# Performance work log

Hardware: AMD Instinct MI355X
Metric: run time of the kernel (lower is better)

Reference implementation:

```python
import jax, jax.numpy as jnp
import numpy as np

B, C, H = 32768, 1000, 128


def setup_inputs() -> dict:
    key = jax.random.key(0)
    ks = jax.random.split(key, 4)
    return {
        "logits": jax.random.normal(ks[0], (B, C), dtype=jnp.float32),
        "W1": jax.random.normal(ks[1], (C, H), dtype=jnp.float32) * 0.02,
        "b1": jnp.zeros((H,), dtype=jnp.float32),
        "W2": jax.random.normal(ks[2], (H, H), dtype=jnp.float32) * 0.02,
        "b2": jnp.zeros((H,), dtype=jnp.float32),
        "W3": jax.random.normal(ks[3], (H, C), dtype=jnp.float32) * 0.02,
        "b3": jnp.zeros((C,), dtype=jnp.float32),
    }


def reference(logits, W1, b1, W2, b2, W3, b3):
    prob = jax.nn.softmax(logits, axis=-1)                      # [B, C]
    # descending sort (torch.sort(descending=True))
    order = jnp.argsort(-prob, axis=-1)                          # [B, C] int
    sorted_prob = jnp.take_along_axis(prob, order, axis=-1)      # [B, C]
    # diffs between consecutive sorted probs, last slot = 1
    diffs = jnp.concatenate(
        [sorted_prob[:, :-1] - sorted_prob[:, 1:],
         jnp.ones((prob.shape[0], 1), dtype=prob.dtype)], axis=1)
    # adapter MLP on prob
    h = jax.nn.relu(prob @ W1 + b1)
    h = jax.nn.relu(h @ W2 + b2)
    cal = h @ W3 + b3                                            # [B, C]
    # sigmoid on all but the last column
    cal = jnp.concatenate([jax.nn.sigmoid(cal[:, :-1]), cal[:, -1:]], axis=1)
    v = diffs * cal                                              # [B, C]
    # S.T @ U @ v  ==  scatter(reverse-cumsum(v)) back to original order
    rev_cumsum = jnp.cumsum(v[:, ::-1], axis=1)[:, ::-1]         # suffix sum
    rows = jnp.arange(logits.shape[0])[:, None]
    fitted = jnp.zeros_like(logits).at[rows, order].set(rev_cumsum)
    return fitted + logits
```

## Files before the change

### kernel.cpp

```cpp
#include <hip/hip_runtime.h>
#include <hip/hip_bf16.h>

#define BROWS 32768
#define CDIM 1000
#define CPAD 1024
#define HDIM 128
#define REG 1056
#define WST  (2 * REG)
#define PHYS(i) ((i) + ((i) >> 5))

typedef __attribute__((ext_vector_type(8))) short short8;
typedef __attribute__((ext_vector_type(4))) float f32x4;

__device__ inline unsigned short f2bf(float x) {
    unsigned int b = __float_as_uint(x);
    unsigned int r = (b + 0x7FFFu + ((b >> 16) & 1u)) >> 16;
    return (unsigned short)r;
}
__device__ inline float bf2f(unsigned short u) {
    return __uint_as_float(((unsigned int)u) << 16);
}

__global__ __launch_bounds__(256) void k_prep(const float* __restrict__ W1,
                                              const float* __restrict__ W2,
                                              const float* __restrict__ W3,
                                              unsigned short* __restrict__ W1t,
                                              unsigned short* __restrict__ W2t,
                                              unsigned short* __restrict__ W3t) {
    const int idx = blockIdx.x * 256 + threadIdx.x;
    {
        const int n = idx >> 10, k = idx & 1023;
        W1t[idx] = (k < CDIM) ? f2bf(W1[(size_t)k * HDIM + n]) : (unsigned short)0;
    }
    {
        const int n = idx >> 7, k = idx & 127;
        W3t[idx] = (n < CDIM) ? f2bf(W3[(size_t)k * CDIM + n]) : (unsigned short)0;
    }
    if (idx < 16384) {
        const int n = idx >> 7, k = idx & 127;
        W2t[idx] = f2bf(W2[(size_t)k * HDIM + n]);
    }
}

__global__ __launch_bounds__(256) void k_softmax(const float* __restrict__ logits,
                                                 unsigned short* __restrict__ prob) {
    const int wv = threadIdx.x >> 6, lane = threadIdx.x & 63;
    const int row = (blockIdx.x << 2) + wv;
    const int base = lane << 4;
    const float* lrow = logits + (size_t)row * CDIM;
    float lg[16];
#pragma unroll
    for (int q = 0; q < 4; ++q) {
        const int c = base + (q << 2);
        if (c < CDIM) {
            const float4 v4 = *reinterpret_cast<const float4*>(lrow + c);
            lg[q * 4] = v4.x; lg[q * 4 + 1] = v4.y; lg[q * 4 + 2] = v4.z; lg[q * 4 + 3] = v4.w;
        } else {
            lg[q * 4] = lg[q * 4 + 1] = lg[q * 4 + 2] = lg[q * 4 + 3] = -INFINITY;
        }
    }
    float mx = lg[0];
#pragma unroll
    for (int e = 1; e < 16; ++e) mx = fmaxf(mx, lg[e]);
#pragma unroll
    for (int off = 32; off >= 1; off >>= 1) mx = fmaxf(mx, __shfl_xor(mx, off));
    float p[16], s = 0.f;
#pragma unroll
    for (int e = 0; e < 16; ++e) { p[e] = __expf(lg[e] - mx); s += p[e]; }
#pragma unroll
    for (int off = 32; off >= 1; off >>= 1) s += __shfl_xor(s, off);
    const float inv = 1.f / s;
    unsigned int w[8];
#pragma unroll
    for (int i = 0; i < 8; ++i) {
        const unsigned int lo = f2bf(p[2 * i] * inv);
        const unsigned int hi = f2bf(p[2 * i + 1] * inv);
        w[i] = lo | (hi << 16);
    }
    uint4 o0, o1;
    o0.x = w[0]; o0.y = w[1]; o0.z = w[2]; o0.w = w[3];
    o1.x = w[4]; o1.y = w[5]; o1.z = w[6]; o1.w = w[7];
    uint4* dst = reinterpret_cast<uint4*>(prob + (size_t)row * CPAD + base);
    dst[0] = o0; dst[1] = o1;
}

template <int EPI>
__global__ __launch_bounds__(512) void k_gemm(const unsigned short* __restrict__ A, int lda,
                                              const unsigned short* __restrict__ Bt, int ldb,
                                              const float* __restrict__ bias,
                                              unsigned short* __restrict__ outp, int ldo,
                                              int K, int nlimit) {
    __shared__ uint4 As[128 * 8];
    __shared__ uint4 Bs[128 * 8];
    const int tid = threadIdx.x;
    const int bm = blockIdx.x, bn = blockIdx.y;
    const int lane = tid & 63, w = tid >> 6;
    const int wm = (w >> 1) << 5;
    const int wn = (w & 1) << 6;
    const int l15 = lane & 15, l4 = lane >> 4;
    f32x4 acc[2][4] = {};

    for (int k0 = 0; k0 < K; k0 += 64) {
        __syncthreads();
#pragma unroll
        for (int i = 0; i < 2; ++i) {
            const int cid = tid + (i << 9);
            const int r = cid >> 3, c = cid & 7;
            As[(r << 3) + (c ^ (r & 7))] =
                *reinterpret_cast<const uint4*>(A + (size_t)(bm * 128 + r) * lda + k0 + (c << 3));
            Bs[(r << 3) + (c ^ (r & 7))] =
                *reinterpret_cast<const uint4*>(Bt + (size_t)(bn * 128 + r) * ldb + k0 + (c << 3));
        }
        __syncthreads();
#pragma unroll
        for (int kk = 0; kk < 2; ++kk) {
            short8 a[2], b[4];
#pragma unroll
            for (int mf = 0; mf < 2; ++mf) {
                const int r = wm + (mf << 4) + l15;
                a[mf] = *reinterpret_cast<const short8*>(&As[(r << 3) + (((kk << 2) + l4) ^ (r & 7))]);
            }
#pragma unroll
            for (int nf = 0; nf < 4; ++nf) {
                const int r = wn + (nf << 4) + l15;
                b[nf] = *reinterpret_cast<const short8*>(&Bs[(r << 3) + (((kk << 2) + l4) ^ (r & 7))]);
            }
#pragma unroll
            for (int mf = 0; mf < 2; ++mf)
#pragma unroll
                for (int nf = 0; nf < 4; ++nf)
                    acc[mf][nf] = __builtin_amdgcn_mfma_f32_16x16x32_bf16(a[mf], b[nf], acc[mf][nf], 0, 0, 0);
        }
    }
#pragma unroll
    for (int mf = 0; mf < 2; ++mf) {
#pragma unroll
        for (int nf = 0; nf < 4; ++nf) {
            const int n = (bn << 7) + wn + (nf << 4) + l15;
            float bv;
            if (EPI == 0) bv = bias[n];
            else bv = (n < nlimit) ? bias[n] : 0.f;
#pragma unroll
            for (int r = 0; r < 4; ++r) {
                const int m = (bm << 7) + wm + (mf << 4) + (l4 << 2) + r;
                float v = acc[mf][nf][r] + bv;
                if (EPI == 0) {
                    v = fmaxf(v, 0.f);
                } else {
                    if (n != nlimit - 1) v = 1.f / (1.f + __expf(-v));
                }
                outp[(size_t)m * ldo + n] = f2bf(v);
            }
        }
    }
}

__global__ __launch_bounds__(256) void k_sortfinish(const float* __restrict__ logits,
                                                    const unsigned short* __restrict__ cal,
                                                    float* __restrict__ out) {
    __shared__ unsigned int shm[4 * WST];
    const int wv = threadIdx.x >> 6, lane = threadIdx.x & 63;
    const int row = (blockIdx.x << 2) + wv;
    unsigned int* smA = &shm[wv * WST];
    unsigned int* smB = smA + REG;
    const int base = lane << 4;
    const int pb = base + (lane >> 1);

#pragma unroll
    for (int e = 0; e < 16; ++e) smA[pb + e] = 0u;

    const float* lrow = logits + (size_t)row * CDIM;
    float lg[16];
#pragma unroll
    for (int q = 0; q < 4; ++q) {
        const int c = base + (q << 2);
        if (c < CDIM) {
            const float4 v4 = *reinterpret_cast<const float4*>(lrow + c);
            lg[q * 4] = v4.x; lg[q * 4 + 1] = v4.y; lg[q * 4 + 2] = v4.z; lg[q * 4 + 3] = v4.w;
        } else {
            lg[q * 4] = lg[q * 4 + 1] = lg[q * 4 + 2] = lg[q * 4 + 3] = -INFINITY;
        }
    }
    const unsigned short* crow = cal + (size_t)row * CPAD + base;
    const uint4 c0v = *reinterpret_cast<const uint4*>(crow);
    const uint4 c1v = *reinterpret_cast<const uint4*>(crow + 8);

    float mx = lg[0];
#pragma unroll
    for (int e = 1; e < 16; ++e) mx = fmaxf(mx, lg[e]);
#pragma unroll
    for (int off = 32; off >= 1; off >>= 1) mx = fmaxf(mx, __shfl_xor(mx, off));
    float p[16], s = 0.f;
#pragma unroll
    for (int e = 0; e < 16; ++e) { p[e] = __expf(lg[e] - mx); s += p[e]; }
#pragma unroll
    for (int off = 32; off >= 1; off >>= 1) s += __shfl_xor(s, off);
    const float inv = 1.f / s;
#pragma unroll
    for (int e = 0; e < 16; ++e) p[e] *= inv;

    unsigned int key[16], offv[16];
#pragma unroll
    for (int e = 0; e < 16; ++e) {
        key[e] = __float_as_uint(p[e]) >> 20;
        offv[e] = (base + e < CDIM) ? atomicAdd(&smA[PHYS(key[e])], 1u) : 0u;
    }

    {
        unsigned int c16[16];
#pragma unroll
        for (int e = 0; e < 16; ++e) c16[e] = smA[pb + e];
        unsigned int lsum = 0;
#pragma unroll
        for (int e = 0; e < 16; ++e) lsum += c16[e];
        unsigned int suf = lsum;
#pragma unroll
        for (int off = 1; off < 64; off <<= 1) {
            const unsigned int u = __shfl_down(suf, off);
            if (lane + off < 64) suf += u;
        }
        unsigned int run = suf - lsum;
        unsigned int st[16];
#pragma unroll
        for (int e = 15; e >= 0; --e) { st[e] = run; run += c16[e]; }
#pragma unroll
        for (int e = 0; e < 16; ++e) smA[pb + e] = st[e];
    }

    int rk[16];
#pragma unroll
    for (int e = 0; e < 16; ++e)
        rk[e] = (base + e < CDIM) ? (int)(smA[PHYS(key[e])] + offv[e]) : 1023;

#pragma unroll
    for (int e = 0; e < 16; ++e)
        if (base + e < CDIM) smB[PHYS(rk[e])] = __float_as_uint(p[e]);

    float sp[16];
#pragma unroll
    for (int e = 0; e < 16; ++e) sp[e] = __uint_as_float(smB[pb + e]);
    const float spn_next = __shfl_down(sp[0], 1);
    const unsigned int cw[8] = {c0v.x, c0v.y, c0v.z, c0v.w, c1v.x, c1v.y, c1v.z, c1v.w};
    float v[16];
#pragma unroll
    for (int e = 0; e < 16; ++e) {
        const int r = base + e;
        const float cv = bf2f((unsigned short)((cw[e >> 1] >> ((e & 1) * 16)) & 0xFFFFu));
        const float spn = (e < 15) ? sp[e + 1] : spn_next;
        float val;
        if (r < CDIM - 1) val = (sp[e] - spn) * cv;
        else if (r == CDIM - 1) val = cv;
        else val = 0.f;
        v[e] = val;
    }
    float lsuf[16], run = 0.f;
#pragma unroll
    for (int e = 15; e >= 0; --e) { run += v[e]; lsuf[e] = run; }
    float pi = run;
#pragma unroll
    for (int off = 1; off < 64; off <<= 1) {
        const float u = __shfl_up(pi, off);
        if (lane >= off) pi += u;
    }
    const float tot = __shfl(pi, 63);
    const float after = tot - pi;

#pragma unroll
    for (int e = 0; e < 16; ++e) smA[pb + e] = __float_as_uint(lsuf[e] + after);
    float f[16];
#pragma unroll
    for (int e = 0; e < 16; ++e) f[e] = __uint_as_float(smA[PHYS(rk[e])]);
#pragma unroll
    for (int q = 0; q < 4; ++q) {
        const int c = base + (q << 2);
        if (c < CDIM) {
            float4 o;
            o.x = lg[q * 4] + f[q * 4];
            o.y = lg[q * 4 + 1] + f[q * 4 + 1];
            o.z = lg[q * 4 + 2] + f[q * 4 + 2];
            o.w = lg[q * 4 + 3] + f[q * 4 + 3];
            *reinterpret_cast<float4*>(out + (size_t)row * CDIM + c) = o;
        }
    }
}

extern "C" void kernel_launch(void* const* d_in, const int* in_sizes, int n_in,
                              void* d_out, int out_size, void* d_ws, size_t ws_size,
                              hipStream_t stream) {
    const float* logits = (const float*)d_in[0];
    const float* W1 = (const float*)d_in[1];
    const float* b1 = (const float*)d_in[2];
    const float* W2 = (const float*)d_in[3];
    const float* b2 = (const float*)d_in[4];
    const float* W3 = (const float*)d_in[5];
    const float* b3 = (const float*)d_in[6];
    float* out = (float*)d_out;

    char* ws = (char*)d_ws;
    unsigned short* prob = (unsigned short*)ws;
    unsigned short* h1   = (unsigned short*)(ws + 67108864);
    unsigned short* h2   = (unsigned short*)(ws + 75497472);
    unsigned short* W1t  = (unsigned short*)(ws + 83886080);
    unsigned short* W2t  = (unsigned short*)(ws + 84148224);
    unsigned short* W3t  = (unsigned short*)(ws + 84180992);
    unsigned short* cal  = prob;

    k_prep<<<512, 256, 0, stream>>>(W1, W2, W3, W1t, W2t, W3t);
    k_softmax<<<BROWS / 4, 256, 0, stream>>>(logits, prob);
    k_gemm<0><<<dim3(BROWS / 128, 1), 512, 0, stream>>>(prob, CPAD, W1t, CPAD, b1, h1, HDIM, CPAD, 0);
    k_gemm<0><<<dim3(BROWS / 128, 1), 512, 0, stream>>>(h1, HDIM, W2t, HDIM, b2, h2, HDIM, HDIM, 0);
    k_gemm<1><<<dim3(BROWS / 128, 8), 512, 0, stream>>>(h2, HDIM, W3t, HDIM, b3, cal, CPAD, HDIM, CDIM);
    k_sortfinish<<<BROWS / 4, 256, 0, stream>>>(logits, cal, out);
}
```

Measured before the change: 177.8 us.

## Fuse softmax into first GEMM A-load and compact calibration buffer

Replaces the softmax kernel that wrote a padded bf16 probability matrix with a row-statistics kernel that stores only the max and inverse sum per row. The first GEMM now reads fp32 logits directly and applies exp, normalize and bf16 conversion while staging A tiles into LDS. This removes the bf16 prob write and re-read at the cost of reading fp32 logits twice and doing more work in the GEMM load phase. The calibration buffer uses an unpadded CDIM stride, and the sort kernel reuses the stored row statistics and shares one LDS region between the histogram and the sorted probabilities, which halves its LDS use.

```diff
diff --git a/kernel.cpp b/kernel.cpp
--- a/kernel.cpp
+++ b/kernel.cpp
@@ -6,7 +6,6 @@
 #define CPAD 1024
 #define HDIM 128
 #define REG 1056
-#define WST  (2 * REG)
 #define PHYS(i) ((i) + ((i) >> 5))
 
 typedef __attribute__((ext_vector_type(8))) short short8;
@@ -42,8 +41,8 @@
     }
 }
 
-__global__ __launch_bounds__(256) void k_softmax(const float* __restrict__ logits,
-                                                 unsigned short* __restrict__ prob) {
+__global__ __launch_bounds__(256) void k_rowstat(const float* __restrict__ logits,
+                                                 float2* __restrict__ rstat) {
     const int wv = threadIdx.x >> 6, lane = threadIdx.x & 63;
     const int row = (blockIdx.x << 2) + wv;
     const int base = lane << 4;
@@ -64,24 +63,100 @@
     for (int e = 1; e < 16; ++e) mx = fmaxf(mx, lg[e]);
 #pragma unroll
     for (int off = 32; off >= 1; off >>= 1) mx = fmaxf(mx, __shfl_xor(mx, off));
-    float p[16], s = 0.f;
-#pragma unroll
-    for (int e = 0; e < 16; ++e) { p[e] = __expf(lg[e] - mx); s += p[e]; }
+    float s = 0.f;
+#pragma unroll
+    for (int e = 0; e < 16; ++e) s += __expf(lg[e] - mx);
 #pragma unroll
     for (int off = 32; off >= 1; off >>= 1) s += __shfl_xor(s, off);
-    const float inv = 1.f / s;
-    unsigned int w[8];
-#pragma unroll
-    for (int i = 0; i < 8; ++i) {
-        const unsigned int lo = f2bf(p[2 * i] * inv);
-        const unsigned int hi = f2bf(p[2 * i + 1] * inv);
-        w[i] = lo | (hi << 16);
-    }
-    uint4 o0, o1;
-    o0.x = w[0]; o0.y = w[1]; o0.z = w[2]; o0.w = w[3];
-    o1.x = w[4]; o1.y = w[5]; o1.z = w[6]; o1.w = w[7];
-    uint4* dst = reinterpret_cast<uint4*>(prob + (size_t)row * CPAD + base);
-    dst[0] = o0; dst[1] = o1;
+    if (lane == 0) rstat[row] = make_float2(mx, 1.f / s);
+}
+
+__global__ __launch_bounds__(512) void k_gemm1f(const float* __restrict__ logits,
+                                                const float2* __restrict__ rstat,
+                                                const unsigned short* __restrict__ W1t,
+                                                const float* __restrict__ b1,
+                                                unsigned short* __restrict__ h1) {
+    __shared__ uint4 As[128 * 8];
+    __shared__ uint4 Bs[128 * 8];
+    const int tid = threadIdx.x;
+    const int bm = blockIdx.x;
+    const int lane = tid & 63, w = tid >> 6;
+    const int wm = (w >> 1) << 5;
+    const int wn = (w & 1) << 6;
+    const int l15 = lane & 15, l4 = lane >> 4;
+    f32x4 acc[2][4] = {};
+
+    const int r = tid >> 2, q4 = tid & 3;
+    const float* lrowS = logits + (size_t)(bm * 128 + r) * CDIM;
+    const float2 st = rstat[bm * 128 + r];
+    const float mxv = st.x, invv = st.y;
+
+    for (int k0 = 0; k0 < CPAD; k0 += 64) {
+        __syncthreads();
+        {
+            unsigned int wd[8];
+#pragma unroll
+            for (int j = 0; j < 4; ++j) {
+                const int c = k0 + (q4 << 4) + (j << 2);
+                float p0 = 0.f, p1 = 0.f, p2 = 0.f, p3 = 0.f;
+                if (c < CDIM) {
+                    const float4 v4 = *reinterpret_cast<const float4*>(lrowS + c);
+                    p0 = __expf(v4.x - mxv) * invv;
+                    p1 = __expf(v4.y - mxv) * invv;
+                    p2 = __expf(v4.z - mxv) * invv;
+                    p3 = __expf(v4.w - mxv) * invv;
+                }
+                wd[2 * j]     = (unsigned int)f2bf(p0) | ((unsigned int)f2bf(p1) << 16);
+                wd[2 * j + 1] = (unsigned int)f2bf(p2) | ((unsigned int)f2bf(p3) << 16);
+            }
+            const int cc = q4 << 1;
+            uint4 u0, u1;
+            u0.x = wd[0]; u0.y = wd[1]; u0.z = wd[2]; u0.w = wd[3];
+            u1.x = wd[4]; u1.y = wd[5]; u1.z = wd[6]; u1.w = wd[7];
+            As[(r << 3) + (cc ^ (r & 7))] = u0;
+            As[(r << 3) + ((cc + 1) ^ (r & 7))] = u1;
+        }
+#pragma unroll
+        for (int i = 0; i < 2; ++i) {
+            const int cid = tid + (i << 9);
+            const int rb = cid >> 3, cb = cid & 7;
+            Bs[(rb << 3) + (cb ^ (rb & 7))] =
+                *reinterpret_cast<const uint4*>(W1t + (size_t)rb * CPAD + k0 + (cb << 3));
+        }
+        __syncthreads();
+#pragma unroll
+        for (int kk = 0; kk < 2; ++kk) {
+            short8 a[2], b[4];
+#pragma unroll
+            for (int mf = 0; mf < 2; ++mf) {
+                const int rr = wm + (mf << 4) + l15;
+                a[mf] = *reinterpret_cast<const short8*>(&As[(rr << 3) + (((kk << 2) + l4) ^ (rr & 7))]);
+            }
+#pragma unroll
+            for (int nf = 0; nf < 4; ++nf) {
+                const int rr = wn + (nf << 4) + l15;
+                b[nf] = *reinterpret_cast<const short8*>(&Bs[(rr << 3) + (((kk << 2) + l4) ^ (rr & 7))]);
+            }
+#pragma unroll
+            for (int mf = 0; mf < 2; ++mf)
+#pragma unroll
+                for (int nf = 0; nf < 4; ++nf)
+                    acc[mf][nf] = __builtin_amdgcn_mfma_f32_16x16x32_bf16(a[mf], b[nf], acc[mf][nf], 0, 0, 0);
+        }
+    }
+#pragma unroll
+    for (int mf = 0; mf < 2; ++mf) {
+#pragma unroll
+        for (int nf = 0; nf < 4; ++nf) {
+            const int n = wn + (nf << 4) + l15;
+            const float bv = b1[n];
+#pragma unroll
+            for (int rr = 0; rr < 4; ++rr) {
+                const int m = (bm << 7) + wm + (mf << 4) + (l4 << 2) + rr;
+                h1[(size_t)m * HDIM + n] = f2bf(fmaxf(acc[mf][nf][rr] + bv, 0.f));
+            }
+        }
+    }
 }
 
 template <int EPI>
@@ -137,9 +212,8 @@
 #pragma unroll
         for (int nf = 0; nf < 4; ++nf) {
             const int n = (bn << 7) + wn + (nf << 4) + l15;
-            float bv;
-            if (EPI == 0) bv = bias[n];
-            else bv = (n < nlimit) ? bias[n] : 0.f;
+            if (EPI == 1 && n >= nlimit) continue;
+            const float bv = bias[n];
 #pragma unroll
             for (int r = 0; r < 4; ++r) {
                 const int m = (bm << 7) + wm + (mf << 4) + (l4 << 2) + r;
@@ -156,13 +230,13 @@
 }
 
 __global__ __launch_bounds__(256) void k_sortfinish(const float* __restrict__ logits,
+                                                    const float2* __restrict__ rstat,
                                                     const unsigned short* __restrict__ cal,
                                                     float* __restrict__ out) {
-    __shared__ unsigned int shm[4 * WST];
+    __shared__ unsigned int shm[4 * REG];
     const int wv = threadIdx.x >> 6, lane = threadIdx.x & 63;
     const int row = (blockIdx.x << 2) + wv;
-    unsigned int* smA = &shm[wv * WST];
-    unsigned int* smB = smA + REG;
+    unsigned int* smA = &shm[wv * REG];
     const int base = lane << 4;
     const int pb = base + (lane >> 1);
 
@@ -181,23 +255,15 @@
             lg[q * 4] = lg[q * 4 + 1] = lg[q * 4 + 2] = lg[q * 4 + 3] = -INFINITY;
         }
     }
-    const unsigned short* crow = cal + (size_t)row * CPAD + base;
+    const unsigned short* crow = cal + (size_t)row * CDIM + base;
     const uint4 c0v = *reinterpret_cast<const uint4*>(crow);
     const uint4 c1v = *reinterpret_cast<const uint4*>(crow + 8);
 
-    float mx = lg[0];
-#pragma unroll
-    for (int e = 1; e < 16; ++e) mx = fmaxf(mx, lg[e]);
-#pragma unroll
-    for (int off = 32; off >= 1; off >>= 1) mx = fmaxf(mx, __shfl_xor(mx, off));
-    float p[16], s = 0.f;
-#pragma unroll
-    for (int e = 0; e < 16; ++e) { p[e] = __expf(lg[e] - mx); s += p[e]; }
-#pragma unroll
-    for (int off = 32; off >= 1; off >>= 1) s += __shfl_xor(s, off);
-    const float inv = 1.f / s;
-#pragma unroll
-    for (int e = 0; e < 16; ++e) p[e] *= inv;
+    const float2 st = rstat[row];
+    const float mx = st.x, inv = st.y;
+    float p[16];
+#pragma unroll
+    for (int e = 0; e < 16; ++e) p[e] = __expf(lg[e] - mx) * inv;
 
     unsigned int key[16], offv[16];
 #pragma unroll
@@ -220,11 +286,11 @@
             if (lane + off < 64) suf += u;
         }
         unsigned int run = suf - lsum;
-        unsigned int st[16];
-#pragma unroll
-        for (int e = 15; e >= 0; --e) { st[e] = run; run += c16[e]; }
-#pragma unroll
-        for (int e = 0; e < 16; ++e) smA[pb + e] = st[e];
+        unsigned int stv[16];
+#pragma unroll
+        for (int e = 15; e >= 0; --e) { stv[e] = run; run += c16[e]; }
+#pragma unroll
+        for (int e = 0; e < 16; ++e) smA[pb + e] = stv[e];
     }
 
     int rk[16];
@@ -234,11 +300,11 @@
 
 #pragma unroll
     for (int e = 0; e < 16; ++e)
-        if (base + e < CDIM) smB[PHYS(rk[e])] = __float_as_uint(p[e]);
+        if (base + e < CDIM) smA[PHYS(rk[e])] = __float_as_uint(p[e]);
 
     float sp[16];
 #pragma unroll
-    for (int e = 0; e < 16; ++e) sp[e] = __uint_as_float(smB[pb + e]);
+    for (int e = 0; e < 16; ++e) sp[e] = __uint_as_float(smA[pb + e]);
     const float spn_next = __shfl_down(sp[0], 1);
     const unsigned int cw[8] = {c0v.x, c0v.y, c0v.z, c0v.w, c1v.x, c1v.y, c1v.z, c1v.w};
     float v[16];
@@ -297,18 +363,18 @@
     float* out = (float*)d_out;
 
     char* ws = (char*)d_ws;
-    unsigned short* prob = (unsigned short*)ws;
-    unsigned short* h1   = (unsigned short*)(ws + 67108864);
-    unsigned short* h2   = (unsigned short*)(ws + 75497472);
-    unsigned short* W1t  = (unsigned short*)(ws + 83886080);
-    unsigned short* W2t  = (unsigned short*)(ws + 84148224);
-    unsigned short* W3t  = (unsigned short*)(ws + 84180992);
-    unsigned short* cal  = prob;
+    float2*         rstat = (float2*)ws;
+    unsigned short* h1    = (unsigned short*)(ws + 262144);
+    unsigned short* h2    = (unsigned short*)(ws + 8650752);
+    unsigned short* cal   = (unsigned short*)(ws + 17039360);
+    unsigned short* W1t   = (unsigned short*)(ws + 82575360);
+    unsigned short* W2t   = (unsigned short*)(ws + 82837504);
+    unsigned short* W3t   = (unsigned short*)(ws + 82870272);
 
     k_prep<<<512, 256, 0, stream>>>(W1, W2, W3, W1t, W2t, W3t);
-    k_softmax<<<BROWS / 4, 256, 0, stream>>>(logits, prob);
-    k_gemm<0><<<dim3(BROWS / 128, 1), 512, 0, stream>>>(prob, CPAD, W1t, CPAD, b1, h1, HDIM, CPAD, 0);
+    k_rowstat<<<BROWS / 4, 256, 0, stream>>>(logits, rstat);
+    k_gemm1f<<<BROWS / 128, 512, 0, stream>>>(logits, rstat, W1t, b1, h1);
     k_gemm<0><<<dim3(BROWS / 128, 1), 512, 0, stream>>>(h1, HDIM, W2t, HDIM, b2, h2, HDIM, HDIM, 0);
-    k_gemm<1><<<dim3(BROWS / 128, 8), 512, 0, stream>>>(h2, HDIM, W3t, HDIM, b3, cal, CPAD, HDIM, CDIM);
-    k_sortfinish<<<BROWS / 4, 256, 0, stream>>>(logits, cal, out);
-}
+    k_gemm<1><<<dim3(BROWS / 128, 8), 512, 0, stream>>>(h2, HDIM, W3t, HDIM, b3, cal, CDIM, HDIM, CDIM);
+    k_sortfinish<<<BROWS / 4, 256, 0, stream>>>(logits, rstat, cal, out);
+}
```

Result: slower. 191.1 us (+7.5%).

## Swizzle sort LDS into one vectorized buffer and store cal unpadded

Applied to the files above, without the earlier changes.

The sort-and-finish kernel replaces its two padded per-wave shared-memory regions with a single 1024-word region per wave. It uses an XOR swizzle so that the contiguous per-lane accesses become uint4 vector loads and stores while bank conflicts stay low, and shared memory per block roughly halves, which may raise occupancy. The calibration output is now written with a row stride of 1000 instead of 1024, and the GEMM epilogue skips the padded columns, cutting memory traffic. The risks are reusing one buffer for counts, sorted probabilities and suffix sums, and the final row's vector load reading a little past the cal buffer into the workspace.

```diff
diff --git a/kernel.cpp b/kernel.cpp
--- a/kernel.cpp
+++ b/kernel.cpp
@@ -5,9 +5,7 @@
 #define CDIM 1000
 #define CPAD 1024
 #define HDIM 128
-#define REG 1056
-#define WST  (2 * REG)
-#define PHYS(i) ((i) + ((i) >> 5))
+#define SWZ(w) ((w) ^ ((((w) >> 5) & 7) << 2))
 
 typedef __attribute__((ext_vector_type(8))) short short8;
 typedef __attribute__((ext_vector_type(4))) float f32x4;
@@ -137,9 +135,8 @@
 #pragma unroll
         for (int nf = 0; nf < 4; ++nf) {
             const int n = (bn << 7) + wn + (nf << 4) + l15;
-            float bv;
-            if (EPI == 0) bv = bias[n];
-            else bv = (n < nlimit) ? bias[n] : 0.f;
+            if (EPI == 1 && n >= nlimit) continue;
+            const float bv = bias[n];
 #pragma unroll
             for (int r = 0; r < 4; ++r) {
                 const int m = (bm << 7) + wm + (mf << 4) + (l4 << 2) + r;
@@ -158,16 +155,21 @@
 __global__ __launch_bounds__(256) void k_sortfinish(const float* __restrict__ logits,
                                                     const unsigned short* __restrict__ cal,
                                                     float* __restrict__ out) {
-    __shared__ unsigned int shm[4 * WST];
+    __shared__ unsigned int shm[4 * 1024];
     const int wv = threadIdx.x >> 6, lane = threadIdx.x & 63;
     const int row = (blockIdx.x << 2) + wv;
-    unsigned int* smA = &shm[wv * WST];
-    unsigned int* smB = smA + REG;
+    unsigned int* sm = &shm[wv << 10];
     const int base = lane << 4;
-    const int pb = base + (lane >> 1);
-
-#pragma unroll
-    for (int e = 0; e < 16; ++e) smA[pb + e] = 0u;
+
+    int cb[4];
+#pragma unroll
+    for (int j = 0; j < 4; ++j) { const int wd = base + (j << 2); cb[j] = SWZ(wd); }
+
+    {
+        uint4 z; z.x = 0; z.y = 0; z.z = 0; z.w = 0;
+#pragma unroll
+        for (int j = 0; j < 4; ++j) *reinterpret_cast<uint4*>(&sm[cb[j]]) = z;
+    }
 
     const float* lrow = logits + (size_t)row * CDIM;
     float lg[16];
@@ -181,7 +183,7 @@
             lg[q * 4] = lg[q * 4 + 1] = lg[q * 4 + 2] = lg[q * 4 + 3] = -INFINITY;
         }
     }
-    const unsigned short* crow = cal + (size_t)row * CPAD + base;
+    const unsigned short* crow = cal + (size_t)row * CDIM + base;
     const uint4 c0v = *reinterpret_cast<const uint4*>(crow);
     const uint4 c1v = *reinterpret_cast<const uint4*>(crow + 8);
 
@@ -199,17 +201,21 @@
 #pragma unroll
     for (int e = 0; e < 16; ++e) p[e] *= inv;
 
-    unsigned int key[16], offv[16];
+    unsigned int offv[16]; int swk[16];
 #pragma unroll
     for (int e = 0; e < 16; ++e) {
-        key[e] = __float_as_uint(p[e]) >> 20;
-        offv[e] = (base + e < CDIM) ? atomicAdd(&smA[PHYS(key[e])], 1u) : 0u;
+        const unsigned int key = __float_as_uint(p[e]) >> 20;
+        swk[e] = SWZ((int)key);
+        offv[e] = (base + e < CDIM) ? atomicAdd(&sm[swk[e]], 1u) : 0u;
     }
 
     {
         unsigned int c16[16];
 #pragma unroll
-        for (int e = 0; e < 16; ++e) c16[e] = smA[pb + e];
+        for (int j = 0; j < 4; ++j) {
+            const uint4 v4 = *reinterpret_cast<const uint4*>(&sm[cb[j]]);
+            c16[4 * j] = v4.x; c16[4 * j + 1] = v4.y; c16[4 * j + 2] = v4.z; c16[4 * j + 3] = v4.w;
+        }
         unsigned int lsum = 0;
 #pragma unroll
         for (int e = 0; e < 16; ++e) lsum += c16[e];
@@ -220,25 +226,35 @@
             if (lane + off < 64) suf += u;
         }
         unsigned int run = suf - lsum;
-        unsigned int st[16];
-#pragma unroll
-        for (int e = 15; e >= 0; --e) { st[e] = run; run += c16[e]; }
-#pragma unroll
-        for (int e = 0; e < 16; ++e) smA[pb + e] = st[e];
-    }
-
-    int rk[16];
+        unsigned int stv[16];
+#pragma unroll
+        for (int e = 15; e >= 0; --e) { stv[e] = run; run += c16[e]; }
+#pragma unroll
+        for (int j = 0; j < 4; ++j) {
+            uint4 v4;
+            v4.x = stv[4 * j]; v4.y = stv[4 * j + 1]; v4.z = stv[4 * j + 2]; v4.w = stv[4 * j + 3];
+            *reinterpret_cast<uint4*>(&sm[cb[j]]) = v4;
+        }
+    }
+
+    int swr[16];
+#pragma unroll
+    for (int e = 0; e < 16; ++e) {
+        const int rk = (base + e < CDIM) ? (int)(sm[swk[e]] + offv[e]) : 1023;
+        swr[e] = SWZ(rk);
+    }
+
 #pragma unroll
     for (int e = 0; e < 16; ++e)
-        rk[e] = (base + e < CDIM) ? (int)(smA[PHYS(key[e])] + offv[e]) : 1023;
-
-#pragma unroll
-    for (int e = 0; e < 16; ++e)
-        if (base + e < CDIM) smB[PHYS(rk[e])] = __float_as_uint(p[e]);
+        if (base + e < CDIM) sm[swr[e]] = __float_as_uint(p[e]);
 
     float sp[16];
 #pragma unroll
-    for (int e = 0; e < 16; ++e) sp[e] = __uint_as_float(smB[pb + e]);
+    for (int j = 0; j < 4; ++j) {
+        const uint4 v4 = *reinterpret_cast<const uint4*>(&sm[cb[j]]);
+        sp[4 * j] = __uint_as_float(v4.x); sp[4 * j + 1] = __uint_as_float(v4.y);
+        sp[4 * j + 2] = __uint_as_float(v4.z); sp[4 * j + 3] = __uint_as_float(v4.w);
+    }
     const float spn_next = __shfl_down(sp[0], 1);
     const unsigned int cw[8] = {c0v.x, c0v.y, c0v.z, c0v.w, c1v.x, c1v.y, c1v.z, c1v.w};
     float v[16];
@@ -266,10 +282,17 @@
     const float after = tot - pi;
 
 #pragma unroll
-    for (int e = 0; e < 16; ++e) smA[pb + e] = __float_as_uint(lsuf[e] + after);
+    for (int j = 0; j < 4; ++j) {
+        uint4 v4;
+        v4.x = __float_as_uint(lsuf[4 * j] + after);
+        v4.y = __float_as_uint(lsuf[4 * j + 1] + after);
+        v4.z = __float_as_uint(lsuf[4 * j + 2] + after);
+        v4.w = __float_as_uint(lsuf[4 * j + 3] + after);
+        *reinterpret_cast<uint4*>(&sm[cb[j]]) = v4;
+    }
     float f[16];
 #pragma unroll
-    for (int e = 0; e < 16; ++e) f[e] = __uint_as_float(smA[PHYS(rk[e])]);
+    for (int e = 0; e < 16; ++e) f[e] = __uint_as_float(sm[swr[e]]);
 #pragma unroll
     for (int q = 0; q < 4; ++q) {
         const int c = base + (q << 2);
@@ -309,6 +332,6 @@
     k_softmax<<<BROWS / 4, 256, 0, stream>>>(logits, prob);
     k_gemm<0><<<dim3(BROWS / 128, 1), 512, 0, stream>>>(prob, CPAD, W1t, CPAD, b1, h1, HDIM, CPAD, 0);
     k_gemm<0><<<dim3(BROWS / 128, 1), 512, 0, stream>>>(h1, HDIM, W2t, HDIM, b2, h2, HDIM, HDIM, 0);
-    k_gemm<1><<<dim3(BROWS / 128, 8), 512, 0, stream>>>(h2, HDIM, W3t, HDIM, b3, cal, CPAD, HDIM, CDIM);
+    k_gemm<1><<<dim3(BROWS / 128, 8), 512, 0, stream>>>(h2, HDIM, W3t, HDIM, b3, cal, CDIM, HDIM, CDIM);
     k_sortfinish<<<BROWS / 4, 256, 0, stream>>>(logits, cal, out);
 }
```

New measurement: 177.5 us. Within noise of the previous version (-0.1%).
